# Performance work log

Measured on AMD Instinct MI355X. Metric: run time of the kernel, lower is better.

Reference implementation:

```python
import jax, jax.numpy as jnp
import numpy as np

N = 50000
IN_DIM = 512
HIDDEN = 64
OUT_DIM = 47
E1 = 800000
E2 = 1200000


def setup_inputs() -> dict:
    key = jax.random.key(0)
    ks = jax.random.split(key, 10)
    x = jax.random.normal(ks[0], (N, IN_DIM), dtype=jnp.float32)
    src1 = jax.random.randint(ks[1], (E1,), 0, N, dtype=jnp.int32)
    dst1 = jax.random.randint(ks[2], (E1,), 0, N, dtype=jnp.int32)
    w1 = jax.random.uniform(ks[3], (E1,), dtype=jnp.float32)
    src2 = jax.random.randint(ks[4], (E2,), 0, N, dtype=jnp.int32)
    dst2 = jax.random.randint(ks[5], (E2,), 0, N, dtype=jnp.int32)
    w2 = jax.random.uniform(ks[6], (E2,), dtype=jnp.float32)
    embed_w = jax.random.normal(ks[7], (IN_DIM, HIDDEN), dtype=jnp.float32) / np.sqrt(IN_DIM)
    embed_b = jnp.zeros((HIDDEN,), dtype=jnp.float32)
    total_dim = (2 ** 3 - 1) * HIDDEN  # k=2 -> 7*hidden
    cls_w = jax.random.normal(ks[8], (total_dim, OUT_DIM), dtype=jnp.float32) / np.sqrt(total_dim)
    cls_b = jnp.zeros((OUT_DIM,), dtype=jnp.float32)
    return {"x": x, "src1": src1, "dst1": dst1, "w1": w1,
            "src2": src2, "dst2": dst2, "w2": w2,
            "embed_w": embed_w, "embed_b": embed_b,
            "cls_w": cls_w, "cls_b": cls_b}


def _spmm(src, dst, w, h, n):
    # out[i] = sum_{e: dst[e]==i} w[e] * h[src[e]]  == sparse_adj @ h
    return jax.ops.segment_sum(w[:, None] * h[src], dst, num_segments=n)


def reference(x, src1, dst1, w1, src2, dst2, w2, embed_w, embed_b, cls_w, cls_b):
    k = 2
    # dropout is identity in eval mode
    h = jax.nn.relu(x @ embed_w + embed_b)  # [N, hidden]
    reps = [h]
    for _ in range(k):
        h1 = _spmm(src1, dst1, w1, h, N)  # strict 1-hop
        h2 = _spmm(src2, dst2, w2, h, N)  # strict 2-hop
        h = jax.nn.relu(jnp.concatenate([h1, h2], axis=1))
        reps.append(h)
    h_final = jnp.concatenate(reps, axis=1)  # [N, 7*hidden]
    return h_final @ cls_w + cls_b
```

## Files before the change

kernel.cpp:

```cpp
#include <hip/hip_runtime.h>

#define N_NODES 50000
#define IN_DIM 512
#define HIDDEN 64
#define OUT_DIM 47
#define HSTRIDE 448

#define NBINS 391
#define CAP1 3072
#define CAP2 4096
#define CHUNK 2048
#define XB 1024

typedef unsigned short u16;
typedef short v8s __attribute__((ext_vector_type(8)));
typedef float v4f __attribute__((ext_vector_type(4)));

union F4 { float4 v; float f[4]; };
union U4 { uint4 v; unsigned u[4]; };

static __device__ __forceinline__ u16 f2bf(float f) {
  unsigned u = __float_as_uint(f);
  u += 0x7fffu + ((u >> 16) & 1u);
  return (u16)(u >> 16);
}
static __device__ __forceinline__ float bf2f(u16 h) {
  return __uint_as_float(((unsigned)h) << 16);
}

__global__ __launch_bounds__(256) void prep(
    const float* __restrict__ embed_w, u16* __restrict__ weTh,
    u16* __restrict__ weTl, const float* __restrict__ cls_w,
    u16* __restrict__ wcTh, u16* __restrict__ wcTl,
    const float* __restrict__ x, u16* __restrict__ x_bf,
    const int* __restrict__ src1, const int* __restrict__ dst1,
    const float* __restrict__ w1, int E1, int c1,
    const int* __restrict__ src2, const int* __restrict__ dst2,
    const float* __restrict__ w2, int E2,
    int* __restrict__ binCursor, int2* __restrict__ stg1,
    int2* __restrict__ stg2) {
  __shared__ int hist[NBINS], sbase[NBINS], cur[NBINS], segrel[NBINS];
  __shared__ int wsum[4];
  __shared__ int2 buf[CHUNK];

  int b = blockIdx.x;
  if (b < 16) {
    int tid = b * 256 + threadIdx.x;
    int col = tid >> 6;
    int k8 = (tid & 63) * 8;
#pragma unroll
    for (int j = 0; j < 8; j++) {
      float v = embed_w[(size_t)(k8 + j) * HIDDEN + col];
      u16 h = f2bf(v);
      weTh[(size_t)col * IN_DIM + k8 + j] = h;
      weTl[(size_t)col * IN_DIM + k8 + j] = f2bf(v - bf2f(h));
    }
    return;
  }
  if (b < 27) {
    int tid = (b - 16) * 256 + threadIdx.x;
    if (tid < 48 * 56) {
      int col = tid / 56;
      int k8 = (tid % 56) * 8;
#pragma unroll
      for (int j = 0; j < 8; j++) {
        float v = (col < OUT_DIM) ? cls_w[(size_t)(k8 + j) * OUT_DIM + col] : 0.f;
        u16 h = f2bf(v);
        wcTh[(size_t)col * HSTRIDE + k8 + j] = h;
        wcTl[(size_t)col * HSTRIDE + k8 + j] = f2bf(v - bf2f(h));
      }
    }
    return;
  }
  if (b < 27 + XB) {
    const float4* x4 = (const float4*)x;
    uint2* o2 = (uint2*)x_bf;
    int i0 = (b - 27) * 256 + threadIdx.x;
    int stride = XB * 256;
    int tot = N_NODES * IN_DIM / 4;
    for (int i = i0; i < tot; i += stride) {
      F4 v;
      v.v = x4[i];
      uint2 o;
      o.x = (unsigned)f2bf(v.f[0]) | ((unsigned)f2bf(v.f[1]) << 16);
      o.y = (unsigned)f2bf(v.f[2]) | ((unsigned)f2bf(v.f[3]) << 16);
      o2[i] = o;
    }
    return;
  }

  int q = b - 27 - XB;
  const int *src, *dst;
  const float* w;
  int E, cap;
  int2* stg;
  int* bc;
  if (q < c1) {
    src = src1; dst = dst1; w = w1; E = E1; stg = stg1; bc = binCursor; cap = CAP1;
  } else {
    q -= c1;
    src = src2; dst = dst2; w = w2; E = E2; stg = stg2; bc = binCursor + NBINS; cap = CAP2;
  }
  int e0 = q * CHUNK;
  int n = E - e0;
  if (n > CHUNK) n = CHUNK;
  int t = threadIdx.x;

  for (int i = t; i < NBINS; i += 256) hist[i] = 0;
  __syncthreads();

  int2 pk[8];
#pragma unroll
  for (int j = 0; j < 8; j++) {
    int idx = t + j * 256;
    if (idx < n) {
      int d = dst[e0 + idx];
      int bin = d >> 7;
      pk[j] = make_int2(src[e0 + idx] | ((d & 127) << 16) | (bin << 23),
                        __float_as_int(w[e0 + idx]));
      atomicAdd(&hist[bin], 1);
    } else {
      pk[j].x = -1;
    }
  }
  __syncthreads();

  int a0 = 0, a1 = 0;
  if (t < 196) {
    a0 = hist[2 * t];
    if (2 * t + 1 < NBINS) a1 = hist[2 * t + 1];
  }
  int s = a0 + a1;
  int lane = t & 63, wid = t >> 6;
  int ps = s;
#pragma unroll
  for (int off = 1; off < 64; off <<= 1) {
    int v = __shfl_up(ps, off, 64);
    if (lane >= off) ps += v;
  }
  if (lane == 63) wsum[wid] = ps;
  __syncthreads();
  if (t == 0) {
    int c = 0;
#pragma unroll
    for (int i = 0; i < 4; i++) { int tmp = wsum[i]; wsum[i] = c; c += tmp; }
  }
  __syncthreads();
  int excl = ps - s + wsum[wid];
  if (t < 196) {
    sbase[2 * t] = excl;
    cur[2 * t] = excl;
    if (2 * t + 1 < NBINS) { sbase[2 * t + 1] = excl + a0; cur[2 * t + 1] = excl + a0; }
  }
  __syncthreads();

#pragma unroll
  for (int j = 0; j < 8; j++) {
    if (pk[j].x != -1) {
      int bin = (pk[j].x >> 23) & 0x1FF;
      int pos = atomicAdd(&cur[bin], 1);
      buf[pos] = pk[j];
    }
  }
  for (int i = t; i < NBINS; i += 256) {
    int h = hist[i];
    segrel[i] = h ? atomicAdd(&bc[i], h) : 0;
  }
  __syncthreads();

  for (int i = t; i < n; i += 256) {
    int2 e = buf[i];
    int bin = (e.x >> 23) & 0x1FF;
    int pos = segrel[bin] + (i - sbase[bin]);
    if (pos < cap)
      stg[(size_t)bin * cap + pos] = make_int2(e.x & 0x7FFFFF, e.y);
  }
}

__global__ __launch_bounds__(512) void binscan(const int* __restrict__ cnt,
                                               int* __restrict__ scanout) {
  const int* in = cnt + blockIdx.x * NBINS;
  int* out = scanout + blockIdx.x * NBINS;
  int tid = threadIdx.x, lane = tid & 63, wid = tid >> 6;
  __shared__ int wsum[8];
  int v0 = (tid < NBINS) ? in[tid] : 0;
  int v = v0;
#pragma unroll
  for (int off = 1; off < 64; off <<= 1) {
    int t = __shfl_up(v, off, 64);
    if (lane >= off) v += t;
  }
  if (lane == 63) wsum[wid] = v;
  __syncthreads();
  if (tid < 8) {
    int s = wsum[tid], sc = s;
#pragma unroll
    for (int off = 1; off < 8; off <<= 1) {
      int t = __shfl_up(sc, off, 8);
      if (tid >= off) sc += t;
    }
    wsum[tid] = sc - s;
  }
  __syncthreads();
  if (tid < NBINS) out[tid] = v - v0 + wsum[wid];
}

__global__ __launch_bounds__(256) void embed_place(
    const u16* __restrict__ x_bf, const u16* __restrict__ wTh,
    const u16* __restrict__ wTl, const float* __restrict__ bias,
    u16* __restrict__ hcat, const int* __restrict__ binCursor,
    const int* __restrict__ binScan, const int2* __restrict__ stg1,
    int2* __restrict__ ew1, int* __restrict__ ep1,
    const int2* __restrict__ stg2, int2* __restrict__ ew2,
    int* __restrict__ ep2) {
  int b = blockIdx.x;
  if (b < 782) {
    int wave = threadIdx.x >> 6, lane = threadIdx.x & 63;
    int row0 = b * 64 + wave * 16;
    int m = lane & 15, kq = lane >> 4;
    int rowA = row0 + m;
    if (rowA >= N_NODES) rowA = N_NODES - 1;
    const u16* xr = x_bf + (size_t)rowA * IN_DIM;

    v4f acc[4];
#pragma unroll
    for (int nf = 0; nf < 4; nf++) acc[nf] = (v4f){0.f, 0.f, 0.f, 0.f};

#pragma unroll 4
    for (int k0 = 0; k0 < IN_DIM; k0 += 32) {
      int kk = k0 + kq * 8;
      v8s a = *(const v8s*)(xr + kk);
#pragma unroll
      for (int nf = 0; nf < 4; nf++) {
        int col = nf * 16 + m;
        v8s bh = *(const v8s*)(wTh + (size_t)col * IN_DIM + kk);
        v8s bl = *(const v8s*)(wTl + (size_t)col * IN_DIM + kk);
        acc[nf] = __builtin_amdgcn_mfma_f32_16x16x32_bf16(a, bh, acc[nf], 0, 0, 0);
        acc[nf] = __builtin_amdgcn_mfma_f32_16x16x32_bf16(a, bl, acc[nf], 0, 0, 0);
      }
    }

#pragma unroll
    for (int nf = 0; nf < 4; nf++) {
      int col = nf * 16 + m;
      float bv = bias[col];
#pragma unroll
      for (int reg = 0; reg < 4; reg++) {
        int rowC = row0 + kq * 4 + reg;
        if (rowC < N_NODES) {
          float v = acc[nf][reg] + bv;
          hcat[(size_t)rowC * HSTRIDE + col] = f2bf(v > 0.f ? v : 0.f);
        }
      }
    }
    return;
  }

  int pb = b - 782;
  int lb = pb < NBINS ? pb : pb - NBINS;
  const int2* stg;
  int2* ew;
  int* ep;
  int cap;
  if (pb < NBINS) { stg = stg1; ew = ew1; ep = ep1; cap = CAP1; }
  else            { stg = stg2; ew = ew2; ep = ep2; cap = CAP2; }
  int cnt = binCursor[pb];
  if (cnt > cap) cnt = cap;
  int base = binScan[pb];
  const int2* seg = stg + (size_t)lb * cap;
  int node0 = lb << 7;
  int nnodes = N_NODES - node0;
  if (nnodes > 128) nnodes = 128;

  __shared__ int ncnt[128], noff[128], ncur[128];
  __shared__ int t0;
  if (threadIdx.x < 128) { ncnt[threadIdx.x] = 0; ncur[threadIdx.x] = 0; }
  __syncthreads();
  for (int t = threadIdx.x; t < cnt; t += 256)
    atomicAdd(&ncnt[(seg[t].x >> 16) & 127], 1);
  __syncthreads();
  int v0 = 0, v = 0;
  if (threadIdx.x < 128) {
    v0 = ncnt[threadIdx.x];
    v = v0;
    int lane = threadIdx.x & 63;
#pragma unroll
    for (int off = 1; off < 64; off <<= 1) {
      int t = __shfl_up(v, off, 64);
      if (lane >= off) v += t;
    }
    if (threadIdx.x == 63) t0 = v;
  }
  __syncthreads();
  if (threadIdx.x < 128) {
    int excl = v - v0 + (threadIdx.x >= 64 ? t0 : 0);
    noff[threadIdx.x] = excl;
    if (threadIdx.x < nnodes) ep[node0 + threadIdx.x] = base + excl + v0;
  }
  __syncthreads();
  for (int t = threadIdx.x; t < cnt; t += 256) {
    int2 pk = seg[t];
    int nl = (pk.x >> 16) & 127;
    int pos = base + noff[nl] + atomicAdd(&ncur[nl], 1);
    ew[pos] = make_int2(pk.x & 0xFFFF, pk.y);
  }
}

__device__ __forceinline__ void bf8_fma(const U4& r, float wt, float* a) {
#pragma unroll
  for (int i = 0; i < 4; i++) {
    a[2 * i]     += wt * __uint_as_float(r.u[i] << 16);
    a[2 * i + 1] += wt * __uint_as_float(r.u[i] & 0xffff0000u);
  }
}

template <int NT>
__global__ __launch_bounds__(256) void gather2(
    const int* __restrict__ ep1, const int2* __restrict__ ew1,
    const int* __restrict__ ep2, const int2* __restrict__ ew2,
    const u16* __restrict__ hin, u16* __restrict__ out1,
    u16* __restrict__ out2, int half_blocks) {
  int b = blockIdx.x;
  const int* ep;
  const int2* ew;
  u16* out;
  if (b < half_blocks) { ep = ep1; ew = ew1; out = out1; }
  else { b -= half_blocks; ep = ep2; ew = ew2; out = out2; }

  int tid = b * 256 + threadIdx.x;
  int node = tid / NT;
  if (node >= N_NODES) return;
  int col0 = (tid % NT) * 8;
  int s = node ? ep[node - 1] : 0;
  int e = ep[node];

  float a0[8], a1[8];
#pragma unroll
  for (int i = 0; i < 8; i++) { a0[i] = 0.f; a1[i] = 0.f; }

  int j = s;
  for (; j + 4 <= e; j += 4) {
    int2 p0 = ew[j], p1 = ew[j + 1], p2 = ew[j + 2], p3 = ew[j + 3];
    U4 r0, r1, r2, r3;
    r0.v = *(const uint4*)(hin + (size_t)p0.x * HSTRIDE + col0);
    r1.v = *(const uint4*)(hin + (size_t)p1.x * HSTRIDE + col0);
    r2.v = *(const uint4*)(hin + (size_t)p2.x * HSTRIDE + col0);
    r3.v = *(const uint4*)(hin + (size_t)p3.x * HSTRIDE + col0);
    bf8_fma(r0, __int_as_float(p0.y), a0);
    bf8_fma(r1, __int_as_float(p1.y), a1);
    bf8_fma(r2, __int_as_float(p2.y), a0);
    bf8_fma(r3, __int_as_float(p3.y), a1);
  }
  for (; j < e; j++) {
    int2 p = ew[j];
    U4 r;
    r.v = *(const uint4*)(hin + (size_t)p.x * HSTRIDE + col0);
    bf8_fma(r, __int_as_float(p.y), a0);
  }

  U4 o;
#pragma unroll
  for (int i = 0; i < 4; i++) {
    float lo = a0[2 * i] + a1[2 * i];
    float hi = a0[2 * i + 1] + a1[2 * i + 1];
    lo = lo > 0.f ? lo : 0.f;
    hi = hi > 0.f ? hi : 0.f;
    o.u[i] = ((unsigned)f2bf(hi) << 16) | (unsigned)f2bf(lo);
  }
  *(uint4*)(out + (size_t)node * HSTRIDE + col0) = o.v;
}

__global__ __launch_bounds__(256) void final_mfma(
    const u16* __restrict__ hcat, const u16* __restrict__ wTh,
    const u16* __restrict__ wTl, const float* __restrict__ bias,
    float* __restrict__ out) {
  int wave = threadIdx.x >> 6, lane = threadIdx.x & 63;
  int row0 = blockIdx.x * 64 + wave * 16;
  int m = lane & 15, kq = lane >> 4;
  int rowA = row0 + m;
  if (rowA >= N_NODES) rowA = N_NODES - 1;
  const u16* hr = hcat + (size_t)rowA * HSTRIDE;

  v4f acc[3];
#pragma unroll
  for (int nf = 0; nf < 3; nf++) acc[nf] = (v4f){0.f, 0.f, 0.f, 0.f};

#pragma unroll 2
  for (int k0 = 0; k0 < HSTRIDE; k0 += 32) {
    int kk = k0 + kq * 8;
    v8s a = *(const v8s*)(hr + kk);
#pragma unroll
    for (int nf = 0; nf < 3; nf++) {
      int col = nf * 16 + m;
      v8s bh = *(const v8s*)(wTh + (size_t)col * HSTRIDE + kk);
      v8s bl = *(const v8s*)(wTl + (size_t)col * HSTRIDE + kk);
      acc[nf] = __builtin_amdgcn_mfma_f32_16x16x32_bf16(a, bh, acc[nf], 0, 0, 0);
      acc[nf] = __builtin_amdgcn_mfma_f32_16x16x32_bf16(a, bl, acc[nf], 0, 0, 0);
    }
  }

#pragma unroll
  for (int nf = 0; nf < 3; nf++) {
    int col = nf * 16 + m;
    if (col < OUT_DIM) {
      float bv = bias[col];
#pragma unroll
      for (int reg = 0; reg < 4; reg++) {
        int rowC = row0 + kq * 4 + reg;
        if (rowC < N_NODES)
          out[(size_t)rowC * OUT_DIM + col] = acc[nf][reg] + bv;
      }
    }
  }
}

extern "C" void kernel_launch(void* const* d_in, const int* in_sizes, int n_in,
                              void* d_out, int out_size, void* d_ws,
                              size_t ws_size, hipStream_t stream) {
  const float* x       = (const float*)d_in[0];
  const int*   src1    = (const int*)d_in[1];
  const int*   dst1    = (const int*)d_in[2];
  const float* w1      = (const float*)d_in[3];
  const int*   src2    = (const int*)d_in[4];
  const int*   dst2    = (const int*)d_in[5];
  const float* w2      = (const float*)d_in[6];
  const float* embed_w = (const float*)d_in[7];
  const float* embed_b = (const float*)d_in[8];
  const float* cls_w   = (const float*)d_in[9];
  const float* cls_b   = (const float*)d_in[10];
  int E1 = in_sizes[1];
  int E2 = in_sizes[4];

  float* ws = (float*)d_ws;
  size_t off = 0;
  u16* hcat = (u16*)(ws + off); off += (size_t)N_NODES * HSTRIDE / 2;
  int2* ew1 = (int2*)(ws + off); off += (size_t)2 * E1;
  int2* ew2 = (int2*)(ws + off); off += (size_t)2 * E2;
  int* ep1 = (int*)(ws + off); off += N_NODES;
  int* ep2 = (int*)(ws + off); off += N_NODES;
  int2* stg1 = (int2*)(ws + off); off += (size_t)2 * NBINS * CAP1;
  int2* stg2 = (int2*)(ws + off); off += (size_t)2 * NBINS * CAP2;
  int* binCursor = (int*)(ws + off); off += 2 * NBINS;
  int* binScan = (int*)(ws + off); off += 2 * NBINS;
  u16* weTh = (u16*)(ws + off); off += 16384;
  u16* weTl = (u16*)(ws + off); off += 16384;
  u16* wcTh = (u16*)(ws + off); off += 10752;
  u16* wcTl = (u16*)(ws + off); off += 10752;
  u16* x_bf = (u16*)(ws + off); off += (size_t)N_NODES * IN_DIM / 2;

  int c1 = (E1 + CHUNK - 1) / CHUNK;
  int c2 = (E2 + CHUNK - 1) / CHUNK;

  hipMemsetAsync(binCursor, 0, 2 * NBINS * sizeof(int), stream);
  prep<<<27 + XB + c1 + c2, 256, 0, stream>>>(
      embed_w, weTh, weTl, cls_w, wcTh, wcTl, x, x_bf,
      src1, dst1, w1, E1, c1, src2, dst2, w2, E2,
      binCursor, stg1, stg2);
  binscan<<<2, 512, 0, stream>>>(binCursor, binScan);
  embed_place<<<782 + 2 * NBINS, 256, 0, stream>>>(
      x_bf, weTh, weTl, embed_b, hcat, binCursor, binScan,
      stg1, ew1, ep1, stg2, ew2, ep2);
  gather2<8><<<3126, 256, 0, stream>>>(ep1, ew1, ep2, ew2, hcat,
                                       hcat + 64, hcat + 128, 1563);
  gather2<16><<<6250, 256, 0, stream>>>(ep1, ew1, ep2, ew2, hcat + 64,
                                        hcat + 192, hcat + 320, 3125);
  final_mfma<<<782, 256, 0, stream>>>(hcat, wcTh, wcTl, cls_b, (float*)d_out);
}
```

Baseline: 271.5 us.

## Fuse second-hop gather with classifier matmul via shared memory tile

The second propagation layer's gather is fused with the final classifier MFMA. Each block of 16 nodes gathers both adjacency lists into a shared-memory tile and then multiplies the full 448-wide concatenated representation by the classifier weights. The intermediate layer-2 output is no longer written to or re-read from global memory, so the hcat row stride shrinks from 448 to 192, which also tightens the rows the gathers fetch. In exchange, only 3 of 4 waves do the MFMA, each block runs a serial gather-then-matmul phase, and there are 16 nodes per block instead of 64 rows per block.

```diff
diff --git a/kernel.cpp b/kernel.cpp
--- a/kernel.cpp
+++ b/kernel.cpp
@@ -4,7 +4,8 @@
 #define IN_DIM 512
 #define HIDDEN 64
 #define OUT_DIM 47
-#define HSTRIDE 448
+#define HST 192
+#define KDIM 448
 
 #define NBINS 391
 #define CAP1 3072
@@ -66,8 +67,8 @@
       for (int j = 0; j < 8; j++) {
         float v = (col < OUT_DIM) ? cls_w[(size_t)(k8 + j) * OUT_DIM + col] : 0.f;
         u16 h = f2bf(v);
-        wcTh[(size_t)col * HSTRIDE + k8 + j] = h;
-        wcTl[(size_t)col * HSTRIDE + k8 + j] = f2bf(v - bf2f(h));
+        wcTh[(size_t)col * KDIM + k8 + j] = h;
+        wcTl[(size_t)col * KDIM + k8 + j] = f2bf(v - bf2f(h));
       }
     }
     return;
@@ -249,7 +250,7 @@
         int rowC = row0 + kq * 4 + reg;
         if (rowC < N_NODES) {
           float v = acc[nf][reg] + bv;
-          hcat[(size_t)rowC * HSTRIDE + col] = f2bf(v > 0.f ? v : 0.f);
+          hcat[(size_t)rowC * HST + col] = f2bf(v > 0.f ? v : 0.f);
         }
       }
     }
@@ -342,10 +343,10 @@
   for (; j + 4 <= e; j += 4) {
     int2 p0 = ew[j], p1 = ew[j + 1], p2 = ew[j + 2], p3 = ew[j + 3];
     U4 r0, r1, r2, r3;
-    r0.v = *(const uint4*)(hin + (size_t)p0.x * HSTRIDE + col0);
-    r1.v = *(const uint4*)(hin + (size_t)p1.x * HSTRIDE + col0);
-    r2.v = *(const uint4*)(hin + (size_t)p2.x * HSTRIDE + col0);
-    r3.v = *(const uint4*)(hin + (size_t)p3.x * HSTRIDE + col0);
+    r0.v = *(const uint4*)(hin + (size_t)p0.x * HST + col0);
+    r1.v = *(const uint4*)(hin + (size_t)p1.x * HST + col0);
+    r2.v = *(const uint4*)(hin + (size_t)p2.x * HST + col0);
+    r3.v = *(const uint4*)(hin + (size_t)p3.x * HST + col0);
     bf8_fma(r0, __int_as_float(p0.y), a0);
     bf8_fma(r1, __int_as_float(p1.y), a1);
     bf8_fma(r2, __int_as_float(p2.y), a0);
@@ -354,7 +355,7 @@
   for (; j < e; j++) {
     int2 p = ew[j];
     U4 r;
-    r.v = *(const uint4*)(hin + (size_t)p.x * HSTRIDE + col0);
+    r.v = *(const uint4*)(hin + (size_t)p.x * HST + col0);
     bf8_fma(r, __int_as_float(p.y), a0);
   }
 
@@ -367,48 +368,90 @@
     hi = hi > 0.f ? hi : 0.f;
     o.u[i] = ((unsigned)f2bf(hi) << 16) | (unsigned)f2bf(lo);
   }
-  *(uint4*)(out + (size_t)node * HSTRIDE + col0) = o.v;
-}
-
-__global__ __launch_bounds__(256) void final_mfma(
+  *(uint4*)(out + (size_t)node * HST + col0) = o.v;
+}
+
+__global__ __launch_bounds__(256) void gather16_final(
+    const int* __restrict__ ep1, const int2* __restrict__ ew1,
+    const int* __restrict__ ep2, const int2* __restrict__ ew2,
     const u16* __restrict__ hcat, const u16* __restrict__ wTh,
     const u16* __restrict__ wTl, const float* __restrict__ bias,
     float* __restrict__ out) {
-  int wave = threadIdx.x >> 6, lane = threadIdx.x & 63;
-  int row0 = blockIdx.x * 64 + wave * 16;
-  int m = lane & 15, kq = lane >> 4;
-  int rowA = row0 + m;
-  if (rowA >= N_NODES) rowA = N_NODES - 1;
-  const u16* hr = hcat + (size_t)rowA * HSTRIDE;
-
-  v4f acc[3];
-#pragma unroll
-  for (int nf = 0; nf < 3; nf++) acc[nf] = (v4f){0.f, 0.f, 0.f, 0.f};
-
-#pragma unroll 2
-  for (int k0 = 0; k0 < HSTRIDE; k0 += 32) {
-    int kk = k0 + kq * 8;
-    v8s a = *(const v8s*)(hr + kk);
-#pragma unroll
-    for (int nf = 0; nf < 3; nf++) {
-      int col = nf * 16 + m;
-      v8s bh = *(const v8s*)(wTh + (size_t)col * HSTRIDE + kk);
-      v8s bl = *(const v8s*)(wTl + (size_t)col * HSTRIDE + kk);
-      acc[nf] = __builtin_amdgcn_mfma_f32_16x16x32_bf16(a, bh, acc[nf], 0, 0, 0);
-      acc[nf] = __builtin_amdgcn_mfma_f32_16x16x32_bf16(a, bl, acc[nf], 0, 0, 0);
-    }
-  }
-
-#pragma unroll
-  for (int nf = 0; nf < 3; nf++) {
-    int col = nf * 16 + m;
+  __shared__ __align__(16) u16 hb[16][264];
+  int node0 = blockIdx.x * 16;
+  int tid = threadIdx.x;
+  int nl = tid >> 4;
+  int cg = (tid & 15) * 8;
+  int node = node0 + nl;
+
+#pragma unroll
+  for (int list = 0; list < 2; list++) {
+    const int* ep = list ? ep2 : ep1;
+    const int2* ew = list ? ew2 : ew1;
+    int s = node ? ep[node - 1] : 0;
+    int e = ep[node];
+
+    float a0[8], a1[8];
+#pragma unroll
+    for (int i = 0; i < 8; i++) { a0[i] = 0.f; a1[i] = 0.f; }
+
+    int j = s;
+    for (; j + 4 <= e; j += 4) {
+      int2 p0 = ew[j], p1 = ew[j + 1], p2 = ew[j + 2], p3 = ew[j + 3];
+      U4 r0, r1, r2, r3;
+      r0.v = *(const uint4*)(hcat + (size_t)p0.x * HST + 64 + cg);
+      r1.v = *(const uint4*)(hcat + (size_t)p1.x * HST + 64 + cg);
+      r2.v = *(const uint4*)(hcat + (size_t)p2.x * HST + 64 + cg);
+      r3.v = *(const uint4*)(hcat + (size_t)p3.x * HST + 64 + cg);
+      bf8_fma(r0, __int_as_float(p0.y), a0);
+      bf8_fma(r1, __int_as_float(p1.y), a1);
+      bf8_fma(r2, __int_as_float(p2.y), a0);
+      bf8_fma(r3, __int_as_float(p3.y), a1);
+    }
+    for (; j < e; j++) {
+      int2 p = ew[j];
+      U4 r;
+      r.v = *(const uint4*)(hcat + (size_t)p.x * HST + 64 + cg);
+      bf8_fma(r, __int_as_float(p.y), a0);
+    }
+
+    U4 o;
+#pragma unroll
+    for (int i = 0; i < 4; i++) {
+      float lo = a0[2 * i] + a1[2 * i];
+      float hi = a0[2 * i + 1] + a1[2 * i + 1];
+      lo = lo > 0.f ? lo : 0.f;
+      hi = hi > 0.f ? hi : 0.f;
+      o.u[i] = ((unsigned)f2bf(hi) << 16) | (unsigned)f2bf(lo);
+    }
+    *(uint4*)(&hb[nl][list * 128 + cg]) = o.v;
+  }
+  __syncthreads();
+
+  int wave = tid >> 6, lane = tid & 63;
+  if (wave < 3) {
+    int m = lane & 15, kq = lane >> 4;
+    int col = wave * 16 + m;
+    v4f acc = (v4f){0.f, 0.f, 0.f, 0.f};
+    const u16* hr = hcat + (size_t)(node0 + m) * HST;
+
+#pragma unroll
+    for (int k0 = 0; k0 < KDIM; k0 += 32) {
+      int kk = k0 + kq * 8;
+      v8s a = (kk < 192) ? *(const v8s*)(hr + kk)
+                         : *(const v8s*)(&hb[m][kk - 192]);
+      v8s bh = *(const v8s*)(wTh + (size_t)col * KDIM + kk);
+      v8s bl = *(const v8s*)(wTl + (size_t)col * KDIM + kk);
+      acc = __builtin_amdgcn_mfma_f32_16x16x32_bf16(a, bh, acc, 0, 0, 0);
+      acc = __builtin_amdgcn_mfma_f32_16x16x32_bf16(a, bl, acc, 0, 0, 0);
+    }
+
     if (col < OUT_DIM) {
       float bv = bias[col];
 #pragma unroll
       for (int reg = 0; reg < 4; reg++) {
-        int rowC = row0 + kq * 4 + reg;
-        if (rowC < N_NODES)
-          out[(size_t)rowC * OUT_DIM + col] = acc[nf][reg] + bv;
+        int row = node0 + kq * 4 + reg;
+        out[(size_t)row * OUT_DIM + col] = acc[reg] + bv;
       }
     }
   }
@@ -433,7 +476,7 @@
 
   float* ws = (float*)d_ws;
   size_t off = 0;
-  u16* hcat = (u16*)(ws + off); off += (size_t)N_NODES * HSTRIDE / 2;
+  u16* hcat = (u16*)(ws + off); off += (size_t)N_NODES * HST / 2;
   int2* ew1 = (int2*)(ws + off); off += (size_t)2 * E1;
   int2* ew2 = (int2*)(ws + off); off += (size_t)2 * E2;
   int* ep1 = (int*)(ws + off); off += N_NODES;
@@ -462,7 +505,6 @@
       stg1, ew1, ep1, stg2, ew2, ep2);
   gather2<8><<<3126, 256, 0, stream>>>(ep1, ew1, ep2, ew2, hcat,
                                        hcat + 64, hcat + 128, 1563);
-  gather2<16><<<6250, 256, 0, stream>>>(ep1, ew1, ep2, ew2, hcat + 64,
-                                        hcat + 192, hcat + 320, 3125);
-  final_mfma<<<782, 256, 0, stream>>>(hcat, wcTh, wcTl, cls_b, (float*)d_out);
-}
+  gather16_final<<<3125, 256, 0, stream>>>(ep1, ew1, ep2, ew2, hcat,
+                                           wcTh, wcTl, cls_b, (float*)d_out);
+}
```

Measured after the change: 260.3 us. -4.1%, faster.
